# Kernel tuning notes

Measured on AMD Instinct MI355X. Metric: run time of the kernel, lower is better.

The kernel has to match this reference:

```python
import jax, jax.numpy as jnp
import numpy as np

SELECTED_CLASSES = 5  # selected_classes init arg; loop body is identical each iteration
EPS = 1e-5            # nn.InstanceNorm2d default eps


def setup_inputs() -> dict:
    key = jax.random.key(0)
    k1, k2, k3 = jax.random.split(key, 3)
    x = jax.random.normal(k1, (8, 256, 128, 128), dtype=jnp.float32)
    masks = jax.random.uniform(k2, (8, 512, 512), dtype=jnp.float32)
    conv_w = jax.random.normal(k3, (1, 3, 7, 7), dtype=jnp.float32) * 0.05  # CFR_branches[0], no bias
    in_gamma = jnp.ones((256,), dtype=jnp.float32)   # InstanceNorm2d affine weight
    in_beta = jnp.zeros((256,), dtype=jnp.float32)   # InstanceNorm2d affine bias
    return {"x": x, "masks": masks, "conv_w": conv_w, "in_gamma": in_gamma, "in_beta": in_beta}


def reference(x, masks, conv_w, in_gamma, in_beta):
    B, C, H, W = x.shape
    m = masks[:, None, :, :] if masks.ndim == 3 else masks  # [B,1,Hm,Wm]
    # F.interpolate(..., size=(H,H), mode='bilinear', align_corners=False) -> half-pixel bilinear
    m = jax.image.resize(m, (B, 1, H, H), method="bilinear")
    mid = x * m                                             # [B,C,H,W]
    avg_out = jnp.mean(mid, axis=1, keepdims=True)          # [B,1,H,W]
    max_out = jnp.max(mid, axis=1, keepdims=True)           # [B,1,H,W]
    atten = jnp.concatenate([avg_out, max_out, m], axis=1)  # [B,3,H,W]
    atten = jax.lax.conv_general_dilated(
        atten, conv_w, window_strides=(1, 1), padding=[(3, 3), (3, 3)],
        dimension_numbers=("NCHW", "OIHW", "NCHW"))        # [B,1,H,W]
    atten = jax.nn.sigmoid(atten)
    out = mid * atten
    # set_class_mask_matrix: kmeans1d is not imported -> except branch -> all-ones mask;
    # Regional_Normalization therefore reduces to InstanceNorm2d(out).
    mu = jnp.mean(out, axis=(2, 3), keepdims=True)
    var = jnp.var(out, axis=(2, 3), keepdims=True)
    rn = (out - mu) * jax.lax.rsqrt(var + EPS)
    rn = rn * in_gamma[None, :, None, None] + in_beta[None, :, None, None]
    # loop over selected_classes produces identical outs (idx stays 0); sum == scale
    return jax.nn.relu(SELECTED_CLASSES * rn)
```

## Files before the change

### kernel.cpp

```cpp
#include <hip/hip_runtime.h>
#include <math.h>

#define BB 8
#define CC 256
#define HH 128
#define WW 128
#define HWP 16384
#define MH 512
#define MW 512
#define NPIX (BB*HWP)

__global__ __launch_bounds__(256) void kmask(const float* __restrict__ masks,
                                             float* __restrict__ m_out) {
    int t = blockIdx.x * 256 + threadIdx.x;
    int j = t & 127, i = (t >> 7) & 127, b = t >> 14;
    const float Wt[8] = {1.f, 3.f, 5.f, 7.f, 7.f, 5.f, 3.f, 1.f};
    const float* mb = masks + (size_t)b * MH * MW;
    int r0 = 4 * i - 2, c0 = 4 * j - 2;
    float sh = 0.f;
    #pragma unroll
    for (int q = 0; q < 8; q++) {
        int c = c0 + q;
        if (c >= 0 && c < MW) sh += Wt[q];
    }
    float sv = 0.f, acc = 0.f;
    #pragma unroll
    for (int p = 0; p < 8; p++) {
        int r = r0 + p;
        if (r < 0 || r >= MH) continue;
        sv += Wt[p];
        const float* row = mb + (size_t)r * MW;
        float ra = 0.f;
        #pragma unroll
        for (int q = 0; q < 8; q++) {
            int c = c0 + q;
            if (c >= 0 && c < MW) ra += Wt[q] * row[c];
        }
        acc += Wt[p] * ra;
    }
    m_out[t] = acc / (sv * sh);
}

__global__ __launch_bounds__(256) void kreduce(const float* __restrict__ x,
                                               float* __restrict__ cs,
                                               float* __restrict__ cm) {
    int bid = blockIdx.x;
    int chunk = bid & 63;
    int g = (bid >> 6) & 1;
    int b = bid >> 7;
    int pix = chunk * 256 + threadIdx.x;
    const float* base = x + ((size_t)b * CC + g * 128) * HWP + pix;
    float s = 0.f, mx = -INFINITY;
    #pragma unroll 8
    for (int c = 0; c < 128; c++) {
        float v = base[(size_t)c * HWP];
        s += v;
        mx = fmaxf(mx, v);
    }
    int o = g * NPIX + b * HWP + pix;
    cs[o] = s;
    cm[o] = mx;
}

__global__ __launch_bounds__(256) void kprep(const float* __restrict__ m,
                                             const float* __restrict__ cs,
                                             const float* __restrict__ cm,
                                             float* __restrict__ avgo,
                                             float* __restrict__ maxo) {
    int t = blockIdx.x * 256 + threadIdx.x;
    float mm = m[t];
    float s = cs[t] + cs[t + NPIX];
    float mxx = fmaxf(cm[t], cm[t + NPIX]);
    avgo[t] = mm * (s * (1.f / 256.f));
    maxo[t] = mm * mxx;
}

__global__ __launch_bounds__(256) void kconv(const float* __restrict__ avgo,
                                             const float* __restrict__ maxo,
                                             const float* __restrict__ m,
                                             const float* __restrict__ cw,
                                             float* __restrict__ wprod) {
    __shared__ float w[147];
    if (threadIdx.x < 147) w[threadIdx.x] = cw[threadIdx.x];
    __syncthreads();
    int t = blockIdx.x * 256 + threadIdx.x;
    int j = t & 127, i = (t >> 7) & 127, b = t >> 14;
    const float* arrs[3] = {avgo, maxo, m};
    float acc = 0.f;
    for (int ch = 0; ch < 3; ch++) {
        const float* a = arrs[ch] + (size_t)b * HWP;
        #pragma unroll
        for (int di = -3; di <= 3; di++) {
            int ii = i + di;
            if (ii < 0 || ii >= HH) continue;
            #pragma unroll
            for (int dj = -3; dj <= 3; dj++) {
                int jj = j + dj;
                if (jj < 0 || jj >= WW) continue;
                acc += w[ch * 49 + (di + 3) * 7 + (dj + 3)] * a[ii * WW + jj];
            }
        }
    }
    float at = 1.f / (1.f + expf(-acc));
    wprod[t] = m[t] * at;
}

__global__ __launch_bounds__(256) void kfinal(const float* __restrict__ x,
                                              const float* __restrict__ wprod,
                                              const float* __restrict__ gamma,
                                              const float* __restrict__ beta,
                                              float* __restrict__ out) {
    int bc = blockIdx.x;
    int b = bc >> 8, c = bc & 255;
    const float4* xp = (const float4*)(x + (size_t)bc * HWP);
    const float4* wp = (const float4*)(wprod + (size_t)b * HWP);
    float4 o[16];
    float s = 0.f, ss = 0.f;
    #pragma unroll
    for (int k = 0; k < 16; k++) {
        int idx = threadIdx.x + k * 256;
        float4 xv = xp[idx];
        float4 wv = wp[idx];
        float4 ov;
        ov.x = xv.x * wv.x;
        ov.y = xv.y * wv.y;
        ov.z = xv.z * wv.z;
        ov.w = xv.w * wv.w;
        o[k] = ov;
        s += ov.x + ov.y + ov.z + ov.w;
        ss += ov.x * ov.x + ov.y * ov.y + ov.z * ov.z + ov.w * ov.w;
    }
    #pragma unroll
    for (int off = 32; off; off >>= 1) {
        s += __shfl_down(s, off, 64);
        ss += __shfl_down(ss, off, 64);
    }
    __shared__ float ls[4], lss[4];
    __shared__ float smu, srs;
    int wave = threadIdx.x >> 6, lane = threadIdx.x & 63;
    if (lane == 0) { ls[wave] = s; lss[wave] = ss; }
    __syncthreads();
    if (threadIdx.x == 0) {
        float S = ls[0] + ls[1] + ls[2] + ls[3];
        float SS = lss[0] + lss[1] + lss[2] + lss[3];
        float mu = S * (1.f / HWP);
        float var = fmaxf(SS * (1.f / HWP) - mu * mu, 0.f);
        smu = mu;
        srs = rsqrtf(var + 1e-5f);
    }
    __syncthreads();
    float mu = smu;
    float g5 = 5.f * srs * gamma[c];
    float b5 = 5.f * beta[c];
    float4* op = (float4*)(out + (size_t)bc * HWP);
    #pragma unroll
    for (int k = 0; k < 16; k++) {
        int idx = threadIdx.x + k * 256;
        float4 ov = o[k], r;
        r.x = fmaxf(fmaf(ov.x - mu, g5, b5), 0.f);
        r.y = fmaxf(fmaf(ov.y - mu, g5, b5), 0.f);
        r.z = fmaxf(fmaf(ov.z - mu, g5, b5), 0.f);
        r.w = fmaxf(fmaf(ov.w - mu, g5, b5), 0.f);
        op[idx] = r;
    }
}

extern "C" void kernel_launch(void* const* d_in, const int* in_sizes, int n_in,
                              void* d_out, int out_size, void* d_ws, size_t ws_size,
                              hipStream_t stream) {
    const float* x      = (const float*)d_in[0];
    const float* masks  = (const float*)d_in[1];
    const float* conv_w = (const float*)d_in[2];
    const float* gamma  = (const float*)d_in[3];
    const float* beta   = (const float*)d_in[4];
    float* out = (float*)d_out;

    float* ws = (float*)d_ws;
    float* m_arr  = ws;
    float* cs     = ws + (size_t)NPIX;
    float* cm     = ws + (size_t)3 * NPIX;
    float* avgo   = ws + (size_t)5 * NPIX;
    float* maxo   = ws + (size_t)6 * NPIX;
    float* wprod  = ws + (size_t)7 * NPIX;

    kmask<<<NPIX / 256, 256, 0, stream>>>(masks, m_arr);
    kreduce<<<1024, 256, 0, stream>>>(x, cs, cm);
    kprep<<<NPIX / 256, 256, 0, stream>>>(m_arr, cs, cm, avgo, maxo);
    kconv<<<NPIX / 256, 256, 0, stream>>>(avgo, maxo, m_arr, conv_w, wprod);
    kfinal<<<BB * CC, 256, 0, stream>>>(x, wprod, gamma, beta, out);
}
```

Baseline: 296.8 us.

## Fuse mask resize with channel reduce, tile conv in shared memory, cut launches

After: 266.4 us. -10.2%, faster.

```diff
diff --git a/kernel.cpp b/kernel.cpp
--- a/kernel.cpp
+++ b/kernel.cpp
@@ -9,107 +9,123 @@
 #define MH 512
 #define MW 512
 #define NPIX (BB*HWP)
-
-__global__ __launch_bounds__(256) void kmask(const float* __restrict__ masks,
-                                             float* __restrict__ m_out) {
-    int t = blockIdx.x * 256 + threadIdx.x;
-    int j = t & 127, i = (t >> 7) & 127, b = t >> 14;
-    const float Wt[8] = {1.f, 3.f, 5.f, 7.f, 7.f, 5.f, 3.f, 1.f};
-    const float* mb = masks + (size_t)b * MH * MW;
-    int r0 = 4 * i - 2, c0 = 4 * j - 2;
-    float sh = 0.f;
-    #pragma unroll
-    for (int q = 0; q < 8; q++) {
-        int c = c0 + q;
-        if (c >= 0 && c < MW) sh += Wt[q];
-    }
-    float sv = 0.f, acc = 0.f;
-    #pragma unroll
-    for (int p = 0; p < 8; p++) {
-        int r = r0 + p;
-        if (r < 0 || r >= MH) continue;
-        sv += Wt[p];
-        const float* row = mb + (size_t)r * MW;
-        float ra = 0.f;
+#define IQ 4096
+
+__global__ __launch_bounds__(256) void k1(const float* __restrict__ masks,
+                                          const float* __restrict__ x,
+                                          float* __restrict__ m_out,
+                                          float* __restrict__ cs,
+                                          float* __restrict__ cm) {
+    int bid = blockIdx.x, tid = threadIdx.x;
+    if ((bid & 1) == 0) {
+        int t = (bid >> 1) * 256 + tid;
+        int j = t & 127, i = (t >> 7) & 127, b = t >> 14;
+        const float Wt[8] = {1.f, 3.f, 5.f, 7.f, 7.f, 5.f, 3.f, 1.f};
+        const float* mb = masks + (size_t)b * (MH * MW);
+        int r0 = 4 * i - 2, c0 = 4 * j - 2;
+        float cwgt[8];
+        int ccl[8];
+        float sh = 0.f;
         #pragma unroll
         for (int q = 0; q < 8; q++) {
             int c = c0 + q;
-            if (c >= 0 && c < MW) ra += Wt[q] * row[c];
-        }
-        acc += Wt[p] * ra;
-    }
-    m_out[t] = acc / (sv * sh);
-}
-
-__global__ __launch_bounds__(256) void kreduce(const float* __restrict__ x,
-                                               float* __restrict__ cs,
-                                               float* __restrict__ cm) {
-    int bid = blockIdx.x;
-    int chunk = bid & 63;
-    int g = (bid >> 6) & 1;
-    int b = bid >> 7;
-    int pix = chunk * 256 + threadIdx.x;
-    const float* base = x + ((size_t)b * CC + g * 128) * HWP + pix;
-    float s = 0.f, mx = -INFINITY;
-    #pragma unroll 8
-    for (int c = 0; c < 128; c++) {
-        float v = base[(size_t)c * HWP];
-        s += v;
-        mx = fmaxf(mx, v);
-    }
-    int o = g * NPIX + b * HWP + pix;
-    cs[o] = s;
-    cm[o] = mx;
-}
-
-__global__ __launch_bounds__(256) void kprep(const float* __restrict__ m,
-                                             const float* __restrict__ cs,
-                                             const float* __restrict__ cm,
-                                             float* __restrict__ avgo,
-                                             float* __restrict__ maxo) {
-    int t = blockIdx.x * 256 + threadIdx.x;
-    float mm = m[t];
-    float s = cs[t] + cs[t + NPIX];
-    float mxx = fmaxf(cm[t], cm[t + NPIX]);
-    avgo[t] = mm * (s * (1.f / 256.f));
-    maxo[t] = mm * mxx;
-}
-
-__global__ __launch_bounds__(256) void kconv(const float* __restrict__ avgo,
-                                             const float* __restrict__ maxo,
-                                             const float* __restrict__ m,
-                                             const float* __restrict__ cw,
-                                             float* __restrict__ wprod) {
+            bool v = (unsigned)c < (unsigned)MW;
+            cwgt[q] = v ? Wt[q] : 0.f;
+            sh += cwgt[q];
+            ccl[q] = min(max(c, 0), MW - 1);
+        }
+        float acc = 0.f, sv = 0.f;
+        #pragma unroll
+        for (int p = 0; p < 8; p++) {
+            int r = r0 + p;
+            bool v = (unsigned)r < (unsigned)MH;
+            float wp = v ? Wt[p] : 0.f;
+            sv += wp;
+            const float* row = mb + (size_t)min(max(r, 0), MH - 1) * MW;
+            float ra = 0.f;
+            #pragma unroll
+            for (int q = 0; q < 8; q++) ra += cwgt[q] * row[ccl[q]];
+            acc += wp * ra;
+        }
+        m_out[t] = acc / (sv * sh);
+    } else {
+        int id = bid >> 1;
+        int chunk = id & 15;
+        int g = (id >> 4) & 3;
+        int b = id >> 6;
+        int qi = chunk * 256 + tid;
+        const float4* xb = (const float4*)x + ((size_t)(b * CC + g * 64)) * IQ + qi;
+        float4 s = {0.f, 0.f, 0.f, 0.f};
+        float4 mx = {-INFINITY, -INFINITY, -INFINITY, -INFINITY};
+        #pragma unroll 8
+        for (int c = 0; c < 64; c++) {
+            float4 v = xb[(size_t)c * IQ];
+            s.x += v.x; s.y += v.y; s.z += v.z; s.w += v.w;
+            mx.x = fmaxf(mx.x, v.x); mx.y = fmaxf(mx.y, v.y);
+            mx.z = fmaxf(mx.z, v.z); mx.w = fmaxf(mx.w, v.w);
+        }
+        size_t o = (size_t)g * (NPIX / 4) + (size_t)b * IQ + qi;
+        ((float4*)cs)[o] = s;
+        ((float4*)cm)[o] = mx;
+    }
+}
+
+#define TW 64
+#define TH 4
+#define IW 70
+#define IH 10
+#define PITCH 72
+__global__ __launch_bounds__(256) void k2(const float* __restrict__ m,
+                                          const float* __restrict__ cs,
+                                          const float* __restrict__ cm,
+                                          const float* __restrict__ cw,
+                                          float* __restrict__ wprod) {
     __shared__ float w[147];
-    if (threadIdx.x < 147) w[threadIdx.x] = cw[threadIdx.x];
+    __shared__ float pa[IH * PITCH], px[IH * PITCH], pm[IH * PITCH];
+    int tid = threadIdx.x, bid = blockIdx.x;
+    int bx = bid & 1, by = (bid >> 1) & 31, b = bid >> 6;
+    if (tid < 147) w[tid] = cw[tid];
+    int ox = bx * TW - 3, oy = by * TH - 3;
+    for (int idx = tid; idx < IW * IH; idx += 256) {
+        int r = idx / IW, c = idx - r * IW;
+        int gi = oy + r, gj = ox + c;
+        float av = 0.f, mxv = 0.f, mv = 0.f;
+        if ((unsigned)gi < (unsigned)HH && (unsigned)gj < (unsigned)WW) {
+            int p = b * HWP + gi * WW + gj;
+            mv = m[p];
+            float s = cs[p] + cs[p + NPIX] + cs[p + 2 * NPIX] + cs[p + 3 * NPIX];
+            float mmx = fmaxf(fmaxf(cm[p], cm[p + NPIX]),
+                              fmaxf(cm[p + 2 * NPIX], cm[p + 3 * NPIX]));
+            av = mv * s * (1.f / 256.f);
+            mxv = mv * mmx;
+        }
+        pa[r * PITCH + c] = av;
+        px[r * PITCH + c] = mxv;
+        pm[r * PITCH + c] = mv;
+    }
     __syncthreads();
-    int t = blockIdx.x * 256 + threadIdx.x;
-    int j = t & 127, i = (t >> 7) & 127, b = t >> 14;
-    const float* arrs[3] = {avgo, maxo, m};
+    int col = tid & 63, r = tid >> 6;
     float acc = 0.f;
-    for (int ch = 0; ch < 3; ch++) {
-        const float* a = arrs[ch] + (size_t)b * HWP;
+    #pragma unroll
+    for (int di = 0; di < 7; di++) {
         #pragma unroll
-        for (int di = -3; di <= 3; di++) {
-            int ii = i + di;
-            if (ii < 0 || ii >= HH) continue;
-            #pragma unroll
-            for (int dj = -3; dj <= 3; dj++) {
-                int jj = j + dj;
-                if (jj < 0 || jj >= WW) continue;
-                acc += w[ch * 49 + (di + 3) * 7 + (dj + 3)] * a[ii * WW + jj];
-            }
+        for (int dj = 0; dj < 7; dj++) {
+            int li = (r + di) * PITCH + col + dj;
+            acc += w[di * 7 + dj] * pa[li];
+            acc += w[49 + di * 7 + dj] * px[li];
+            acc += w[98 + di * 7 + dj] * pm[li];
         }
     }
     float at = 1.f / (1.f + expf(-acc));
-    wprod[t] = m[t] * at;
-}
-
-__global__ __launch_bounds__(256) void kfinal(const float* __restrict__ x,
-                                              const float* __restrict__ wprod,
-                                              const float* __restrict__ gamma,
-                                              const float* __restrict__ beta,
-                                              float* __restrict__ out) {
+    float res = pm[(r + 3) * PITCH + col + 3] * at;
+    wprod[b * HWP + (by * TH + r) * WW + bx * TW + col] = res;
+}
+
+__global__ __launch_bounds__(256) void k3(const float* __restrict__ x,
+                                          const float* __restrict__ wprod,
+                                          const float* __restrict__ gamma,
+                                          const float* __restrict__ beta,
+                                          float* __restrict__ out) {
     int bc = blockIdx.x;
     int b = bc >> 8, c = bc & 255;
     const float4* xp = (const float4*)(x + (size_t)bc * HWP);
@@ -122,10 +138,8 @@
         float4 xv = xp[idx];
         float4 wv = wp[idx];
         float4 ov;
-        ov.x = xv.x * wv.x;
-        ov.y = xv.y * wv.y;
-        ov.z = xv.z * wv.z;
-        ov.w = xv.w * wv.w;
+        ov.x = xv.x * wv.x; ov.y = xv.y * wv.y;
+        ov.z = xv.z * wv.z; ov.w = xv.w * wv.w;
         o[k] = ov;
         s += ov.x + ov.y + ov.z + ov.w;
         ss += ov.x * ov.x + ov.y * ov.y + ov.z * ov.z + ov.w * ov.w;
@@ -176,16 +190,12 @@
     float* out = (float*)d_out;
 
     float* ws = (float*)d_ws;
-    float* m_arr  = ws;
-    float* cs     = ws + (size_t)NPIX;
-    float* cm     = ws + (size_t)3 * NPIX;
-    float* avgo   = ws + (size_t)5 * NPIX;
-    float* maxo   = ws + (size_t)6 * NPIX;
-    float* wprod  = ws + (size_t)7 * NPIX;
-
-    kmask<<<NPIX / 256, 256, 0, stream>>>(masks, m_arr);
-    kreduce<<<1024, 256, 0, stream>>>(x, cs, cm);
-    kprep<<<NPIX / 256, 256, 0, stream>>>(m_arr, cs, cm, avgo, maxo);
-    kconv<<<NPIX / 256, 256, 0, stream>>>(avgo, maxo, m_arr, conv_w, wprod);
-    kfinal<<<BB * CC, 256, 0, stream>>>(x, wprod, gamma, beta, out);
-}
+    float* m_arr = ws;
+    float* cs    = ws + (size_t)NPIX;
+    float* cm    = ws + (size_t)5 * NPIX;
+    float* wprod = ws + (size_t)9 * NPIX;
+
+    k1<<<1024, 256, 0, stream>>>(masks, x, m_arr, cs, cm);
+    k2<<<512, 256, 0, stream>>>(m_arr, cs, cm, conv_w, wprod);
+    k3<<<BB * CC, 256, 0, stream>>>(x, wprod, gamma, beta, out);
+}
```
